# Kernel optimization log

Hardware: AMD Instinct MI355X
Metric: run time of the kernel (lower is better)

The kernel has to match this reference:

```python
import jax, jax.numpy as jnp
import numpy as np

N_NODES = 1048576
N_EDGES = 16777216
N_GRAPHS = 64
K_HOPS = 4


def setup_inputs() -> dict:
    key = jax.random.key(0)
    k1, k2, k3 = jax.random.split(key, 3)
    x = jax.random.normal(k1, (N_NODES, 1), dtype=jnp.float32)
    edge_index = jax.random.randint(k2, (2, N_EDGES), 0, N_NODES, dtype=jnp.int64)
    W = jax.random.normal(k3, (1, 1), dtype=jnp.float32)
    b = jnp.zeros((1,), dtype=jnp.float32)
    return {"x": x, "edge_index": edge_index, "W": W, "b": b, "num_graphs": N_GRAPHS}


def _sgconv(x, edge_index, W, b, k):
    # PyG SGConv: x <- (D^-1/2 (A + I) D^-1/2)^k x, then linear.
    n = x.shape[0]
    loops = jnp.arange(n, dtype=edge_index.dtype)
    row = jnp.concatenate([edge_index[0], loops])  # source nodes
    col = jnp.concatenate([edge_index[1], loops])  # target nodes
    ones = jnp.ones(row.shape[0], dtype=x.dtype)
    deg = jax.ops.segment_sum(ones, col, num_segments=n)  # in-degree incl. self loop
    dinv = jnp.where(deg > 0, jax.lax.rsqrt(deg), 0.0)
    norm = dinv[row] * dinv[col]  # [E+N]
    for _ in range(k):
        x = jax.ops.segment_sum(norm[:, None] * x[row], col, num_segments=n)
    return x @ W.T + b


def reference(x, edge_index, W, b, num_graphs):
    h = _sgconv(x, edge_index, W, b, K_HOPS)  # [N, 1]
    n = h.shape[0]
    # tensor_split into num_graphs equal chunks (N divisible by num_graphs), mean each
    out = h.reshape(num_graphs, n // num_graphs, 1).mean(axis=1)  # [B, 1]
    return out
```

## Files before the change

### kernel.cpp

```cpp
#include <hip/hip_runtime.h>
#include <stdint.h>

#define N_NODES  (1u << 20)
#define N_EDGES  (1u << 24)
#define N_GRAPHS 64
#define CHUNK    (N_NODES / N_GRAPHS)
#define K_HOPS   4

#define NBUCKET  1024
#define CPB      1024
#define CAP      18432

#define NBLK_SS  512
#define TB_SS    1024
#define EPT      32
#define EPB_SS   (TB_SS * EPT)

#define RBITS    9
#define NRANGE   (1 << RBITS)

typedef uint32_t u32x4 __attribute__((ext_vector_type(4)));
typedef unsigned long long u64x2 __attribute__((ext_vector_type(2)));

__device__ __forceinline__ u32x4 nt_load_u32x4(const uint32_t* p) {
    return __builtin_nontemporal_load((const u32x4*)p);
}
__device__ __forceinline__ u64x2 nt_load_u64x2(const unsigned long long* p) {
    return __builtin_nontemporal_load((const u64x2*)p);
}
__device__ __forceinline__ void nt_store_u32x4(uint32_t* p, u32x4 v) {
    __builtin_nontemporal_store(v, (u32x4*)p);
}

__global__ __launch_bounds__(TB_SS, 4)
void scatter_sort_kernel(const void* __restrict__ ei,
                         int* __restrict__ cursor, uint32_t* __restrict__ packed) {
    __shared__ uint32_t sorted[EPB_SS];
    __shared__ int h[NBUCKET];
    __shared__ int o[NBUCKET];
    __shared__ int ostart[NBUCKET];
    __shared__ int gbase[NBUCKET];
    __shared__ int s_is64;
    int blk = blockIdx.x, tid = threadIdx.x;
    h[tid] = 0;
    size_t base = (size_t)blk * EPB_SS;

    if (tid < 64) {
        size_t widx = 2 * base + 2 * (size_t)tid * 512 + 1;
        int nz = (((const uint32_t*)ei)[widx] != 0u);
        unsigned long long m = __ballot(nz);
        if (tid == 0) s_is64 = (m == 0ull) ? 1 : 0;
    }
    __syncthreads();
    int is64 = s_is64;
    uint32_t c_[EPT];

    if (is64) {
        const unsigned long long* cp = (const unsigned long long*)ei + N_EDGES + base;
        #pragma unroll
        for (int it = 0; it < EPT / 4; ++it) {
            size_t i = (size_t)it * (TB_SS * 4) + (size_t)tid * 4;
            u64x2 a = nt_load_u64x2(cp + i);
            u64x2 b2 = nt_load_u64x2(cp + i + 2);
            c_[it * 4 + 0] = (uint32_t)a.x;  c_[it * 4 + 1] = (uint32_t)a.y;
            c_[it * 4 + 2] = (uint32_t)b2.x; c_[it * 4 + 3] = (uint32_t)b2.y;
            atomicAdd(&h[c_[it * 4 + 0] >> 10], 1);
            atomicAdd(&h[c_[it * 4 + 1] >> 10], 1);
            atomicAdd(&h[c_[it * 4 + 2] >> 10], 1);
            atomicAdd(&h[c_[it * 4 + 3] >> 10], 1);
        }
    } else {
        const uint32_t* cp = (const uint32_t*)ei + N_EDGES + base;
        #pragma unroll
        for (int it = 0; it < EPT / 4; ++it) {
            size_t i = (size_t)it * (TB_SS * 4) + (size_t)tid * 4;
            u32x4 a = nt_load_u32x4(cp + i);
            c_[it * 4 + 0] = a.x; c_[it * 4 + 1] = a.y;
            c_[it * 4 + 2] = a.z; c_[it * 4 + 3] = a.w;
            atomicAdd(&h[a.x >> 10], 1);
            atomicAdd(&h[a.y >> 10], 1);
            atomicAdd(&h[a.z >> 10], 1);
            atomicAdd(&h[a.w >> 10], 1);
        }
    }
    __syncthreads();

    if (tid < 64) {
        int b16 = tid * 16;
        int s = 0;
        #pragma unroll
        for (int j = 0; j < 16; ++j) s += h[b16 + j];
        int v = s;
        #pragma unroll
        for (int off = 1; off < 64; off <<= 1) {
            int up = __shfl_up(v, off, 64);
            if (tid >= off) v += up;
        }
        int run = v - s;
        #pragma unroll
        for (int j = 0; j < 16; ++j) {
            o[b16 + j] = run;
            ostart[b16 + j] = run;
            run += h[b16 + j];
        }
    }
    __syncthreads();

    gbase[tid] = atomicAdd(&cursor[tid], h[tid]);

    if (is64) {
        const unsigned long long* rp = (const unsigned long long*)ei + base;
        #pragma unroll
        for (int it = 0; it < EPT / 4; ++it) {
            size_t i = (size_t)it * (TB_SS * 4) + (size_t)tid * 4;
            u64x2 a = nt_load_u64x2(rp + i);
            u64x2 b2 = nt_load_u64x2(rp + i + 2);
            uint32_t r0 = (uint32_t)a.x, r1 = (uint32_t)a.y;
            uint32_t r2 = (uint32_t)b2.x, r3 = (uint32_t)b2.y;
            { uint32_t c = c_[it * 4 + 0]; int pos = atomicAdd(&o[c >> 10], 1); sorted[pos] = (r0 << 10) | (c & 1023u); }
            { uint32_t c = c_[it * 4 + 1]; int pos = atomicAdd(&o[c >> 10], 1); sorted[pos] = (r1 << 10) | (c & 1023u); }
            { uint32_t c = c_[it * 4 + 2]; int pos = atomicAdd(&o[c >> 10], 1); sorted[pos] = (r2 << 10) | (c & 1023u); }
            { uint32_t c = c_[it * 4 + 3]; int pos = atomicAdd(&o[c >> 10], 1); sorted[pos] = (r3 << 10) | (c & 1023u); }
        }
    } else {
        const uint32_t* rp = (const uint32_t*)ei + base;
        #pragma unroll
        for (int it = 0; it < EPT / 4; ++it) {
            size_t i = (size_t)it * (TB_SS * 4) + (size_t)tid * 4;
            u32x4 a = nt_load_u32x4(rp + i);
            { uint32_t c = c_[it * 4 + 0]; int pos = atomicAdd(&o[c >> 10], 1); sorted[pos] = (a.x << 10) | (c & 1023u); }
            { uint32_t c = c_[it * 4 + 1]; int pos = atomicAdd(&o[c >> 10], 1); sorted[pos] = (a.y << 10) | (c & 1023u); }
            { uint32_t c = c_[it * 4 + 2]; int pos = atomicAdd(&o[c >> 10], 1); sorted[pos] = (a.z << 10) | (c & 1023u); }
            { uint32_t c = c_[it * 4 + 3]; int pos = atomicAdd(&o[c >> 10], 1); sorted[pos] = (a.w << 10) | (c & 1023u); }
        }
    }
    __syncthreads();

    int wave = tid >> 6, lane = tid & 63;
    for (int k = 0; k < NBUCKET / 16; ++k) {
        int b = wave * (NBUCKET / 16) + k;
        int st = ostart[b];
        int len = o[b] - st;
        int gb = gbase[b];
        if (gb + len > CAP) len = CAP - gb > 0 ? CAP - gb : 0;
        uint32_t* dst = packed + (size_t)b * CAP + gb;
        for (int j = lane; j < len; j += 64)
            dst[j] = sorted[st + j];
    }
}

__global__ __launch_bounds__(512, 2)
void degdinv_sort_kernel(uint32_t* __restrict__ packed, const int* __restrict__ cursor,
                         const float* __restrict__ x,
                         float* __restrict__ dinv, float* __restrict__ z) {
    __shared__ uint32_t sbuf[CAP];
    __shared__ int h[CPB];
    __shared__ int ro[NRANGE];
    int b = blockIdx.x, tid = threadIdx.x;
    for (int l = tid; l < CPB; l += 512) h[l] = 0;
    for (int l = tid; l < NRANGE; l += 512) ro[l] = 0;
    __syncthreads();
    int cnt = cursor[b]; if (cnt > CAP) cnt = CAP;
    uint32_t* seg = packed + (size_t)b * CAP;
    int nq = cnt >> 2;

    for (int g = tid; g < nq; g += 512) {
        u32x4 v = *(const u32x4*)(seg + 4 * (size_t)g);
        atomicAdd(&h[v.x & 1023u], 1); atomicAdd(&ro[v.x >> 21], 1);
        atomicAdd(&h[v.y & 1023u], 1); atomicAdd(&ro[v.y >> 21], 1);
        atomicAdd(&h[v.z & 1023u], 1); atomicAdd(&ro[v.z >> 21], 1);
        atomicAdd(&h[v.w & 1023u], 1); atomicAdd(&ro[v.w >> 21], 1);
    }
    {
        int t = (nq << 2) + tid;
        if (t < cnt) { uint32_t p = seg[t]; atomicAdd(&h[p & 1023u], 1); atomicAdd(&ro[p >> 21], 1); }
    }
    __syncthreads();

    if (tid < 64) {
        int b8 = tid * 8;
        int s = 0;
        #pragma unroll
        for (int j = 0; j < 8; ++j) s += ro[b8 + j];
        int v = s;
        #pragma unroll
        for (int off = 1; off < 64; off <<= 1) {
            int up = __shfl_up(v, off, 64);
            if (tid >= off) v += up;
        }
        int run = v - s;
        #pragma unroll
        for (int j = 0; j < 8; ++j) { int c = ro[b8 + j]; ro[b8 + j] = run; run += c; }
    }
    __syncthreads();

    for (int g = tid; g < nq; g += 512) {
        u32x4 v = *(const u32x4*)(seg + 4 * (size_t)g);
        { int p = atomicAdd(&ro[v.x >> 21], 1); sbuf[p] = v.x; }
        { int p = atomicAdd(&ro[v.y >> 21], 1); sbuf[p] = v.y; }
        { int p = atomicAdd(&ro[v.z >> 21], 1); sbuf[p] = v.z; }
        { int p = atomicAdd(&ro[v.w >> 21], 1); sbuf[p] = v.w; }
    }
    {
        int t = (nq << 2) + tid;
        if (t < cnt) { uint32_t p = seg[t]; int q = atomicAdd(&ro[p >> 21], 1); sbuf[q] = p; }
    }
    __syncthreads();

    for (int g = tid; g < nq; g += 512) {
        u32x4 o4;
        o4.x = sbuf[4 * g + 0]; o4.y = sbuf[4 * g + 1];
        o4.z = sbuf[4 * g + 2]; o4.w = sbuf[4 * g + 3];
        nt_store_u32x4(seg + 4 * (size_t)g, o4);
    }
    {
        int t = (nq << 2) + tid;
        if (t < cnt) __builtin_nontemporal_store(sbuf[t], seg + t);
    }
    for (int l = tid; l < CPB; l += 512) {
        int v = b * CPB + l;
        float d = (float)(1.0 / sqrt((double)(h[l] + 1)));
        dinv[v] = d;
        z[v] = d * x[v];
    }
}

__global__ __launch_bounds__(512)
void hop_kernel(const uint32_t* __restrict__ packed, const int* __restrict__ cursor,
                const float* __restrict__ z, const float* __restrict__ dinv,
                float* __restrict__ out) {
    __shared__ float facc[CPB];
    int b = blockIdx.x, tid = threadIdx.x;
    for (int l = tid; l < CPB; l += 512) facc[l] = 0.0f;
    __syncthreads();
    int cnt = cursor[b]; if (cnt > CAP) cnt = CAP;
    const uint32_t* seg = packed + (size_t)b * CAP;
    int nq = cnt >> 2;
    int g = tid;
    for (; g + 1536 < nq; g += 2048) {
        u32x4 q[4];
        q[0] = nt_load_u32x4(seg + 4 * (size_t)g);
        q[1] = nt_load_u32x4(seg + 4 * ((size_t)g + 512));
        q[2] = nt_load_u32x4(seg + 4 * ((size_t)g + 1024));
        q[3] = nt_load_u32x4(seg + 4 * ((size_t)g + 1536));
        float zv[16];
        #pragma unroll
        for (int j = 0; j < 4; ++j) {
            zv[4 * j + 0] = z[q[j].x >> 10];
            zv[4 * j + 1] = z[q[j].y >> 10];
            zv[4 * j + 2] = z[q[j].z >> 10];
            zv[4 * j + 3] = z[q[j].w >> 10];
        }
        #pragma unroll
        for (int j = 0; j < 4; ++j) {
            atomicAdd(&facc[q[j].x & 1023u], zv[4 * j + 0]);
            atomicAdd(&facc[q[j].y & 1023u], zv[4 * j + 1]);
            atomicAdd(&facc[q[j].z & 1023u], zv[4 * j + 2]);
            atomicAdd(&facc[q[j].w & 1023u], zv[4 * j + 3]);
        }
    }
    for (; g < nq; g += 512) {
        u32x4 v = nt_load_u32x4(seg + 4 * (size_t)g);
        float z0 = z[v.x >> 10];
        float z1 = z[v.y >> 10];
        float z2 = z[v.z >> 10];
        float z3 = z[v.w >> 10];
        atomicAdd(&facc[v.x & 1023u], z0);
        atomicAdd(&facc[v.y & 1023u], z1);
        atomicAdd(&facc[v.z & 1023u], z2);
        atomicAdd(&facc[v.w & 1023u], z3);
    }
    int t = (nq << 2) + tid;
    if (t < cnt) { uint32_t p = seg[t]; atomicAdd(&facc[p & 1023u], z[p >> 10]); }
    __syncthreads();
    for (int l = tid; l < CPB; l += 512) {
        int v = b * CPB + l;
        float tt = z[v] + facc[l];
        float d = dinv[v];
        out[v] = d * d * tt;
    }
}

__global__ __launch_bounds__(512)
void hop_final_kernel(const uint32_t* __restrict__ packed, const int* __restrict__ cursor,
                      const float* __restrict__ z, const float* __restrict__ dinv,
                      float* __restrict__ gsum) {
    __shared__ float facc[CPB];
    __shared__ double sdata[8];
    int b = blockIdx.x, tid = threadIdx.x;
    for (int l = tid; l < CPB; l += 512) facc[l] = 0.0f;
    __syncthreads();
    int cnt = cursor[b]; if (cnt > CAP) cnt = CAP;
    const uint32_t* seg = packed + (size_t)b * CAP;
    int nq = cnt >> 2;
    int g = tid;
    for (; g + 1536 < nq; g += 2048) {
        u32x4 q[4];
        q[0] = nt_load_u32x4(seg + 4 * (size_t)g);
        q[1] = nt_load_u32x4(seg + 4 * ((size_t)g + 512));
        q[2] = nt_load_u32x4(seg + 4 * ((size_t)g + 1024));
        q[3] = nt_load_u32x4(seg + 4 * ((size_t)g + 1536));
        float zv[16];
        #pragma unroll
        for (int j = 0; j < 4; ++j) {
            zv[4 * j + 0] = z[q[j].x >> 10];
            zv[4 * j + 1] = z[q[j].y >> 10];
            zv[4 * j + 2] = z[q[j].z >> 10];
            zv[4 * j + 3] = z[q[j].w >> 10];
        }
        #pragma unroll
        for (int j = 0; j < 4; ++j) {
            atomicAdd(&facc[q[j].x & 1023u], zv[4 * j + 0]);
            atomicAdd(&facc[q[j].y & 1023u], zv[4 * j + 1]);
            atomicAdd(&facc[q[j].z & 1023u], zv[4 * j + 2]);
            atomicAdd(&facc[q[j].w & 1023u], zv[4 * j + 3]);
        }
    }
    for (; g < nq; g += 512) {
        u32x4 v = nt_load_u32x4(seg + 4 * (size_t)g);
        float z0 = z[v.x >> 10];
        float z1 = z[v.y >> 10];
        float z2 = z[v.z >> 10];
        float z3 = z[v.w >> 10];
        atomicAdd(&facc[v.x & 1023u], z0);
        atomicAdd(&facc[v.y & 1023u], z1);
        atomicAdd(&facc[v.z & 1023u], z2);
        atomicAdd(&facc[v.w & 1023u], z3);
    }
    int t = (nq << 2) + tid;
    if (t < cnt) { uint32_t p = seg[t]; atomicAdd(&facc[p & 1023u], z[p >> 10]); }
    __syncthreads();
    double s = 0.0;
    for (int l = tid; l < CPB; l += 512) {
        int v = b * CPB + l;
        s += (double)(dinv[v] * (z[v] + facc[l]));
    }
    #pragma unroll
    for (int off = 32; off > 0; off >>= 1) s += __shfl_down(s, off, 64);
    int wave = tid >> 6, lane = tid & 63;
    if (lane == 0) sdata[wave] = s;
    __syncthreads();
    if (tid == 0) {
        double tot = 0.0;
        #pragma unroll
        for (int w = 0; w < 8; ++w) tot += sdata[w];
        atomicAdd(&gsum[b >> 4], (float)tot);
    }
}

__global__ void finalize_kernel(const float* __restrict__ gsum,
                                const float* __restrict__ W, const float* __restrict__ b,
                                float* __restrict__ out) {
    int g = threadIdx.x;
    if (g < N_GRAPHS)
        out[g] = (float)((double)W[0] * ((double)gsum[g] / (double)CHUNK) + (double)b[0]);
}

__global__ void detect_kernel(const uint32_t* __restrict__ ei, int* __restrict__ flag) {
    __shared__ int any_nz;
    if (threadIdx.x == 0) any_nz = 0;
    __syncthreads();
    int nz = 0;
    for (int i = threadIdx.x; i < 32768; i += blockDim.x)
        nz |= (ei[2 * i + 1] != 0u);
    if (nz) atomicOr(&any_nz, 1);
    __syncthreads();
    if (threadIdx.x == 0) flag[0] = any_nz ? 0 : 1;
}

__global__ void zero_int_kernel(int* __restrict__ p) {
    int i = blockIdx.x * blockDim.x + threadIdx.x;
    p[i] = 0;
}

__device__ __forceinline__ int load_idx(const void* ei, int is64, size_t pos) {
    if (is64) return (int)((const unsigned long long*)ei)[pos];
    return ((const int*)ei)[pos];
}

__global__ void count_kernel(const void* __restrict__ ei, const int* __restrict__ flag,
                             int* __restrict__ deg) {
    int e = blockIdx.x * blockDim.x + threadIdx.x;
    int c = load_idx(ei, flag[0], (size_t)N_EDGES + (size_t)e);
    atomicAdd(&deg[c], 1);
}

__global__ void dinv_kernel(const int* __restrict__ deg, float* __restrict__ dinv) {
    int v = blockIdx.x * blockDim.x + threadIdx.x;
    dinv[v] = (float)(1.0 / sqrt((double)(deg[v] + 1)));
}

__global__ void prep_first2_kernel(const float* __restrict__ x, const float* __restrict__ dinv,
                                   float* __restrict__ z, float* __restrict__ acc) {
    int v = blockIdx.x * blockDim.x + threadIdx.x;
    float t = dinv[v] * x[v];
    z[v] = t;
    acc[v] = t;
}

__global__ void prep_mid_kernel(const float* __restrict__ dinv,
                                float* __restrict__ z, float* __restrict__ acc) {
    int v = blockIdx.x * blockDim.x + threadIdx.x;
    float d = dinv[v];
    float t = d * d * acc[v];
    z[v] = t;
    acc[v] = t;
}

__global__ void push_kernel(const void* __restrict__ ei, const int* __restrict__ flag,
                            const float* __restrict__ z, float* __restrict__ acc) {
    int e = blockIdx.x * blockDim.x + threadIdx.x;
    int is64 = flag[0];
    int r, c;
    if (is64) {
        const unsigned long long* p = (const unsigned long long*)ei;
        r = (int)p[e];
        c = (int)p[(size_t)N_EDGES + (size_t)e];
    } else {
        const int* p = (const int*)ei;
        r = p[e];
        c = p[(size_t)N_EDGES + (size_t)e];
    }
    __hip_atomic_fetch_add(&acc[c], z[r], __ATOMIC_RELAXED, __HIP_MEMORY_SCOPE_AGENT);
}

__global__ void final_scale_kernel(const float* __restrict__ dinv,
                                   const float* __restrict__ acc, float* __restrict__ xf) {
    int v = blockIdx.x * blockDim.x + threadIdx.x;
    xf[v] = dinv[v] * acc[v];
}

__global__ void pool_kernel(const float* __restrict__ xf,
                            const float* __restrict__ W, const float* __restrict__ b,
                            float* __restrict__ out) {
    __shared__ double sdata[256];
    int g = blockIdx.x;
    int base = g * CHUNK;
    double s = 0.0;
    for (int i = threadIdx.x; i < CHUNK; i += 256) s += (double)xf[base + i];
    sdata[threadIdx.x] = s;
    __syncthreads();
    for (int off = 128; off > 0; off >>= 1) {
        if (threadIdx.x < off) sdata[threadIdx.x] += sdata[threadIdx.x + off];
        __syncthreads();
    }
    if (threadIdx.x == 0)
        out[g] = (float)((double)W[0] * (sdata[0] / (double)CHUNK) + (double)b[0]);
}

extern "C" void kernel_launch(void* const* d_in, const int* in_sizes, int n_in,
                              void* d_out, int out_size, void* d_ws, size_t ws_size,
                              hipStream_t stream) {
    const float* x = (const float*)d_in[0];
    const void*  ei = d_in[1];
    const float* W = (const float*)d_in[2];
    const float* b = (const float*)d_in[3];
    float* out = (float*)d_out;

    char* ws = (char*)d_ws;
    const size_t MB4 = 4ull << 20;
    size_t off_cursor = 0;
    size_t off_gsum   = NBUCKET * 4;
    size_t off_dinv   = off_gsum + 256;
    size_t off_za     = off_dinv + MB4;
    size_t off_zb     = off_za + MB4;
    size_t off_packed = off_zb + MB4;
    size_t needed     = off_packed + (size_t)NBUCKET * CAP * 4;

    const int TB = 256;

    if (ws_size >= needed) {
        int*      cursor = (int*)(ws + off_cursor);
        float*    gsum   = (float*)(ws + off_gsum);
        float*    dinv   = (float*)(ws + off_dinv);
        float*    za     = (float*)(ws + off_za);
        float*    zb     = (float*)(ws + off_zb);
        uint32_t* packed = (uint32_t*)(ws + off_packed);

        hipMemsetAsync(ws, 0, NBUCKET * 4 + 256, stream);

        scatter_sort_kernel<<<NBLK_SS, TB_SS, 0, stream>>>(ei, cursor, packed);
        degdinv_sort_kernel<<<NBUCKET, 512, 0, stream>>>(packed, cursor, x, dinv, za);

        hop_kernel<<<NBUCKET, 512, 0, stream>>>(packed, cursor, za, dinv, zb);
        hop_kernel<<<NBUCKET, 512, 0, stream>>>(packed, cursor, zb, dinv, za);
        hop_kernel<<<NBUCKET, 512, 0, stream>>>(packed, cursor, za, dinv, zb);
        hop_final_kernel<<<NBUCKET, 512, 0, stream>>>(packed, cursor, zb, dinv, gsum);

        finalize_kernel<<<1, 64, 0, stream>>>(gsum, W, b, out);
    } else {
        int*   flag = (int*)ws;
        float* dinv = (float*)(ws + 256);
        float* za   = (float*)(ws + 256 + MB4);
        float* zb   = (float*)(ws + 256 + 2 * MB4);
        int*   deg  = (int*)(ws + 256 + 3 * MB4);

        detect_kernel<<<1, TB, 0, stream>>>((const uint32_t*)ei, flag);
        zero_int_kernel<<<N_NODES / TB, TB, 0, stream>>>(deg);
        count_kernel<<<N_EDGES / TB, TB, 0, stream>>>(ei, flag, deg);
        dinv_kernel<<<N_NODES / TB, TB, 0, stream>>>(deg, dinv);

        prep_first2_kernel<<<N_NODES / TB, TB, 0, stream>>>(x, dinv, za, zb);
        push_kernel<<<N_EDGES / TB, TB, 0, stream>>>(ei, flag, za, zb);
        for (int h = 1; h < K_HOPS; ++h) {
            prep_mid_kernel<<<N_NODES / TB, TB, 0, stream>>>(dinv, za, zb);
            push_kernel<<<N_EDGES / TB, TB, 0, stream>>>(ei, flag, za, zb);
        }
        final_scale_kernel<<<N_NODES / TB, TB, 0, stream>>>(dinv, zb, za);
        pool_kernel<<<N_GRAPHS, TB, 0, stream>>>(za, W, b, out);
    }
}
```

Measured before the change: 628.8 us.

## Shard hop gather by source range with 16-bucket shared accumulators and merge pass

```diff
diff --git a/kernel.cpp b/kernel.cpp
--- a/kernel.cpp
+++ b/kernel.cpp
@@ -19,8 +19,16 @@
 #define RBITS    9
 #define NRANGE   (1 << RBITS)
 
+#define NB2      64
+#define BPG      16
+#define FACC2    (BPG * CPB)
+#define RS       8
+#define RPS      (NRANGE / RS)
+#define NBLK_HOP (NB2 * RS)
+
 typedef uint32_t u32x4 __attribute__((ext_vector_type(4)));
 typedef unsigned long long u64x2 __attribute__((ext_vector_type(2)));
+typedef float f32x4 __attribute__((ext_vector_type(4)));
 
 __device__ __forceinline__ u32x4 nt_load_u32x4(const uint32_t* p) {
     return __builtin_nontemporal_load((const u32x4*)p);
@@ -30,6 +38,12 @@
 }
 __device__ __forceinline__ void nt_store_u32x4(uint32_t* p, u32x4 v) {
     __builtin_nontemporal_store(v, (u32x4*)p);
+}
+__device__ __forceinline__ void nt_store_f32x4(float* p, f32x4 v) {
+    __builtin_nontemporal_store(v, (f32x4*)p);
+}
+__device__ __forceinline__ f32x4 nt_load_f32x4(const float* p) {
+    return __builtin_nontemporal_load((const f32x4*)p);
 }
 
 __global__ __launch_bounds__(TB_SS, 4)
@@ -152,7 +166,8 @@
 __global__ __launch_bounds__(512, 2)
 void degdinv_sort_kernel(uint32_t* __restrict__ packed, const int* __restrict__ cursor,
                          const float* __restrict__ x,
-                         float* __restrict__ dinv, float* __restrict__ z) {
+                         float* __restrict__ dinv, float* __restrict__ z,
+                         int* __restrict__ rstart) {
     __shared__ uint32_t sbuf[CAP];
     __shared__ int h[CPB];
     __shared__ int ro[NRANGE];
@@ -194,6 +209,10 @@
     }
     __syncthreads();
 
+    for (int l = tid; l < NRANGE; l += 512)
+        rstart[(size_t)b * NRANGE + l] = ro[l];
+    __syncthreads();
+
     for (int g = tid; g < nq; g += 512) {
         u32x4 v = *(const u32x4*)(seg + 4 * (size_t)g);
         { int p = atomicAdd(&ro[v.x >> 21], 1); sbuf[p] = v.x; }
@@ -217,6 +236,132 @@
         int t = (nq << 2) + tid;
         if (t < cnt) __builtin_nontemporal_store(sbuf[t], seg + t);
     }
+    for (int l = tid; l < CPB; l += 512) {
+        int v = b * CPB + l;
+        float d = (float)(1.0 / sqrt((double)(h[l] + 1)));
+        dinv[v] = d;
+        z[v] = d * x[v];
+    }
+}
+
+__global__ __launch_bounds__(512)
+void hop_shard_kernel(const uint32_t* __restrict__ packed, const int* __restrict__ cursor,
+                      const int* __restrict__ rstart, const float* __restrict__ z,
+                      float* __restrict__ P) {
+    __shared__ float facc[FACC2];
+    __shared__ int offs[BPG][RPS + 1];
+    int blk = blockIdx.x, tid = threadIdx.x;
+    int s = blk & (RS - 1), b2 = blk >> 3;
+    for (int l = tid; l < FACC2; l += 512) facc[l] = 0.0f;
+    for (int idx = tid; idx < BPG * (RPS + 1); idx += 512) {
+        int bb = idx / (RPS + 1), r = idx - bb * (RPS + 1);
+        int b = b2 * BPG + bb;
+        int rr = s * RPS + r;
+        int v;
+        if (rr < NRANGE) v = rstart[(size_t)b * NRANGE + rr];
+        else { int c = cursor[b]; v = c > CAP ? CAP : c; }
+        offs[bb][r] = v;
+    }
+    __syncthreads();
+    int wave = tid >> 6, lane = tid & 63;
+    for (int rr = 0; rr < RPS; ++rr) {
+        #pragma unroll
+        for (int k = 0; k < 2; ++k) {
+            int bb = wave * 2 + k;
+            const uint32_t* seg = packed + (size_t)(b2 * BPG + bb) * CAP;
+            int st = offs[bb][rr], en = offs[bb][rr + 1];
+            for (int j = st + lane; j < en; j += 64) {
+                uint32_t e = __builtin_nontemporal_load(seg + j);
+                atomicAdd(&facc[(bb << 10) | (e & 1023u)], z[e >> 10]);
+            }
+        }
+    }
+    __syncthreads();
+    float* Pb = P + (size_t)blk * FACC2;
+    for (int l = tid; l < FACC2 / 4; l += 512) {
+        f32x4 v;
+        v.x = facc[4 * l + 0]; v.y = facc[4 * l + 1];
+        v.z = facc[4 * l + 2]; v.w = facc[4 * l + 3];
+        nt_store_f32x4(Pb + 4 * l, v);
+    }
+}
+
+__global__ __launch_bounds__(512)
+void merge_mid_kernel(const float* __restrict__ P, const float* __restrict__ z,
+                      const float* __restrict__ dinv, float* __restrict__ out) {
+    int i = blockIdx.x * 512 + threadIdx.x;
+    int v0 = i << 2;
+    int b2 = v0 >> 14, c = v0 & (FACC2 - 1);
+    const float* base = P + (size_t)b2 * RS * FACC2 + c;
+    f32x4 acc = {0.0f, 0.0f, 0.0f, 0.0f};
+    #pragma unroll
+    for (int s = 0; s < RS; ++s)
+        acc += nt_load_f32x4(base + (size_t)s * FACC2);
+    f32x4 zz = *(const f32x4*)(z + v0);
+    f32x4 dd = *(const f32x4*)(dinv + v0);
+    f32x4 r = dd * dd * (zz + acc);
+    *(f32x4*)(out + v0) = r;
+}
+
+__global__ __launch_bounds__(512)
+void merge_final_kernel(const float* __restrict__ P, const float* __restrict__ z,
+                        const float* __restrict__ dinv, float* __restrict__ gsum) {
+    __shared__ double sdata[8];
+    int blk = blockIdx.x;
+    int g = blk >> 3, part = blk & 7;
+    int c0 = part * 2048 + (int)threadIdx.x * 4;
+    int v0 = (g << 14) | c0;
+    const float* base = P + (size_t)g * RS * FACC2 + c0;
+    f32x4 acc = {0.0f, 0.0f, 0.0f, 0.0f};
+    #pragma unroll
+    for (int s = 0; s < RS; ++s)
+        acc += nt_load_f32x4(base + (size_t)s * FACC2);
+    f32x4 zz = *(const f32x4*)(z + v0);
+    f32x4 dd = *(const f32x4*)(dinv + v0);
+    f32x4 val = dd * (zz + acc);
+    double sl = (double)val.x + (double)val.y + (double)val.z + (double)val.w;
+    #pragma unroll
+    for (int off = 32; off > 0; off >>= 1) sl += __shfl_down(sl, off, 64);
+    int wave = threadIdx.x >> 6, lane = threadIdx.x & 63;
+    if (lane == 0) sdata[wave] = sl;
+    __syncthreads();
+    if (threadIdx.x == 0) {
+        double tot = 0.0;
+        #pragma unroll
+        for (int w = 0; w < 8; ++w) tot += sdata[w];
+        atomicAdd(&gsum[g], (float)tot);
+    }
+}
+
+__global__ void finalize_kernel(const float* __restrict__ gsum,
+                                const float* __restrict__ W, const float* __restrict__ b,
+                                float* __restrict__ out) {
+    int g = threadIdx.x;
+    if (g < N_GRAPHS)
+        out[g] = (float)((double)W[0] * ((double)gsum[g] / (double)CHUNK) + (double)b[0]);
+}
+
+__global__ __launch_bounds__(512)
+void degdinv_kernel(const uint32_t* __restrict__ packed, const int* __restrict__ cursor,
+                    const float* __restrict__ x,
+                    float* __restrict__ dinv, float* __restrict__ z) {
+    __shared__ int h[CPB];
+    int b = blockIdx.x, tid = threadIdx.x;
+    for (int l = tid; l < CPB; l += 512) h[l] = 0;
+    __syncthreads();
+    int cnt = cursor[b]; if (cnt > CAP) cnt = CAP;
+    const uint32_t* seg = packed + (size_t)b * CAP;
+    int nq = cnt >> 2;
+    for (int g = tid; g < nq; g += 512) {
+        u32x4 v = nt_load_u32x4(seg + g * 4);
+        atomicAdd(&h[v.x & 1023u], 1);
+        atomicAdd(&h[v.y & 1023u], 1);
+        atomicAdd(&h[v.z & 1023u], 1);
+        atomicAdd(&h[v.w & 1023u], 1);
+    }
+    int t = (nq << 2) + tid;
+    if (t < cnt) atomicAdd(&h[seg[t] & 1023u], 1);
+    __syncthreads();
     for (int l = tid; l < CPB; l += 512) {
         int v = b * CPB + l;
         float d = (float)(1.0 / sqrt((double)(h[l] + 1)));
@@ -236,30 +381,7 @@
     int cnt = cursor[b]; if (cnt > CAP) cnt = CAP;
     const uint32_t* seg = packed + (size_t)b * CAP;
     int nq = cnt >> 2;
-    int g = tid;
-    for (; g + 1536 < nq; g += 2048) {
-        u32x4 q[4];
-        q[0] = nt_load_u32x4(seg + 4 * (size_t)g);
-        q[1] = nt_load_u32x4(seg + 4 * ((size_t)g + 512));
-        q[2] = nt_load_u32x4(seg + 4 * ((size_t)g + 1024));
-        q[3] = nt_load_u32x4(seg + 4 * ((size_t)g + 1536));
-        float zv[16];
-        #pragma unroll
-        for (int j = 0; j < 4; ++j) {
-            zv[4 * j + 0] = z[q[j].x >> 10];
-            zv[4 * j + 1] = z[q[j].y >> 10];
-            zv[4 * j + 2] = z[q[j].z >> 10];
-            zv[4 * j + 3] = z[q[j].w >> 10];
-        }
-        #pragma unroll
-        for (int j = 0; j < 4; ++j) {
-            atomicAdd(&facc[q[j].x & 1023u], zv[4 * j + 0]);
-            atomicAdd(&facc[q[j].y & 1023u], zv[4 * j + 1]);
-            atomicAdd(&facc[q[j].z & 1023u], zv[4 * j + 2]);
-            atomicAdd(&facc[q[j].w & 1023u], zv[4 * j + 3]);
-        }
-    }
-    for (; g < nq; g += 512) {
+    for (int g = tid; g < nq; g += 512) {
         u32x4 v = nt_load_u32x4(seg + 4 * (size_t)g);
         float z0 = z[v.x >> 10];
         float z1 = z[v.y >> 10];
@@ -293,30 +415,7 @@
     int cnt = cursor[b]; if (cnt > CAP) cnt = CAP;
     const uint32_t* seg = packed + (size_t)b * CAP;
     int nq = cnt >> 2;
-    int g = tid;
-    for (; g + 1536 < nq; g += 2048) {
-        u32x4 q[4];
-        q[0] = nt_load_u32x4(seg + 4 * (size_t)g);
-        q[1] = nt_load_u32x4(seg + 4 * ((size_t)g + 512));
-        q[2] = nt_load_u32x4(seg + 4 * ((size_t)g + 1024));
-        q[3] = nt_load_u32x4(seg + 4 * ((size_t)g + 1536));
-        float zv[16];
-        #pragma unroll
-        for (int j = 0; j < 4; ++j) {
-            zv[4 * j + 0] = z[q[j].x >> 10];
-            zv[4 * j + 1] = z[q[j].y >> 10];
-            zv[4 * j + 2] = z[q[j].z >> 10];
-            zv[4 * j + 3] = z[q[j].w >> 10];
-        }
-        #pragma unroll
-        for (int j = 0; j < 4; ++j) {
-            atomicAdd(&facc[q[j].x & 1023u], zv[4 * j + 0]);
-            atomicAdd(&facc[q[j].y & 1023u], zv[4 * j + 1]);
-            atomicAdd(&facc[q[j].z & 1023u], zv[4 * j + 2]);
-            atomicAdd(&facc[q[j].w & 1023u], zv[4 * j + 3]);
-        }
-    }
-    for (; g < nq; g += 512) {
+    for (int g = tid; g < nq; g += 512) {
         u32x4 v = nt_load_u32x4(seg + 4 * (size_t)g);
         float z0 = z[v.x >> 10];
         float z1 = z[v.y >> 10];
@@ -346,14 +445,6 @@
         for (int w = 0; w < 8; ++w) tot += sdata[w];
         atomicAdd(&gsum[b >> 4], (float)tot);
     }
-}
-
-__global__ void finalize_kernel(const float* __restrict__ gsum,
-                                const float* __restrict__ W, const float* __restrict__ b,
-                                float* __restrict__ out) {
-    int g = threadIdx.x;
-    if (g < N_GRAPHS)
-        out[g] = (float)((double)W[0] * ((double)gsum[g] / (double)CHUNK) + (double)b[0]);
 }
 
 __global__ void detect_kernel(const uint32_t* __restrict__ ei, int* __restrict__ flag) {
@@ -459,28 +550,65 @@
 
     char* ws = (char*)d_ws;
     const size_t MB4 = 4ull << 20;
+    const size_t packed_sz = (size_t)NBUCKET * CAP * 4;
+    const size_t rstart_sz = (size_t)NBUCKET * NRANGE * 4;
+    const size_t P_sz      = (size_t)NBLK_HOP * FACC2 * 4;
+
     size_t off_cursor = 0;
     size_t off_gsum   = NBUCKET * 4;
     size_t off_dinv   = off_gsum + 256;
     size_t off_za     = off_dinv + MB4;
     size_t off_zb     = off_za + MB4;
-    size_t off_packed = off_zb + MB4;
-    size_t needed     = off_packed + (size_t)NBUCKET * CAP * 4;
+    size_t off_rstart = off_zb + MB4;
+    size_t off_P      = off_rstart + rstart_sz;
+    size_t off_packed2 = off_P + P_sz;
+    size_t needed_v2  = off_packed2 + packed_sz;
+
+    size_t off_packed1 = off_zb + MB4;
+    size_t needed_v1   = off_packed1 + packed_sz;
 
     const int TB = 256;
 
-    if (ws_size >= needed) {
+    if (ws_size >= needed_v2) {
         int*      cursor = (int*)(ws + off_cursor);
         float*    gsum   = (float*)(ws + off_gsum);
         float*    dinv   = (float*)(ws + off_dinv);
         float*    za     = (float*)(ws + off_za);
         float*    zb     = (float*)(ws + off_zb);
-        uint32_t* packed = (uint32_t*)(ws + off_packed);
+        int*      rstart = (int*)(ws + off_rstart);
+        float*    P      = (float*)(ws + off_P);
+        uint32_t* packed = (uint32_t*)(ws + off_packed2);
 
         hipMemsetAsync(ws, 0, NBUCKET * 4 + 256, stream);
 
         scatter_sort_kernel<<<NBLK_SS, TB_SS, 0, stream>>>(ei, cursor, packed);
-        degdinv_sort_kernel<<<NBUCKET, 512, 0, stream>>>(packed, cursor, x, dinv, za);
+        degdinv_sort_kernel<<<NBUCKET, 512, 0, stream>>>(packed, cursor, x, dinv, za, rstart);
+
+        hop_shard_kernel<<<NBLK_HOP, 512, 0, stream>>>(packed, cursor, rstart, za, P);
+        merge_mid_kernel<<<N_NODES / 2048, 512, 0, stream>>>(P, za, dinv, zb);
+
+        hop_shard_kernel<<<NBLK_HOP, 512, 0, stream>>>(packed, cursor, rstart, zb, P);
+        merge_mid_kernel<<<N_NODES / 2048, 512, 0, stream>>>(P, zb, dinv, za);
+
+        hop_shard_kernel<<<NBLK_HOP, 512, 0, stream>>>(packed, cursor, rstart, za, P);
+        merge_mid_kernel<<<N_NODES / 2048, 512, 0, stream>>>(P, za, dinv, zb);
+
+        hop_shard_kernel<<<NBLK_HOP, 512, 0, stream>>>(packed, cursor, rstart, zb, P);
+        merge_final_kernel<<<NBLK_HOP, 512, 0, stream>>>(P, zb, dinv, gsum);
+
+        finalize_kernel<<<1, 64, 0, stream>>>(gsum, W, b, out);
+    } else if (ws_size >= needed_v1) {
+        int*      cursor = (int*)(ws + off_cursor);
+        float*    gsum   = (float*)(ws + off_gsum);
+        float*    dinv   = (float*)(ws + off_dinv);
+        float*    za     = (float*)(ws + off_za);
+        float*    zb     = (float*)(ws + off_zb);
+        uint32_t* packed = (uint32_t*)(ws + off_packed1);
+
+        hipMemsetAsync(ws, 0, NBUCKET * 4 + 256, stream);
+
+        scatter_sort_kernel<<<NBLK_SS, TB_SS, 0, stream>>>(ei, cursor, packed);
+        degdinv_kernel<<<NBUCKET, 512, 0, stream>>>(packed, cursor, x, dinv, za);
 
         hop_kernel<<<NBUCKET, 512, 0, stream>>>(packed, cursor, za, dinv, zb);
         hop_kernel<<<NBUCKET, 512, 0, stream>>>(packed, cursor, zb, dinv, za);
```

Measured after the change: 846.0 us. 1.35x slower.
